# Kernel tuning notes

Hardware: AMD Instinct MI355X
Metric: run time of the kernel (lower is better)

## Reference

```python
import jax, jax.numpy as jnp
import numpy as np
import math

E = 16          # num_experts
TOP_K = 2       # num_experts_per_tok (used as capacity_factor in EC routing)
D = 1024        # embed_dim
F = 4096        # expert_hidden_dim = mlp_ratio * D
SH = 2048       # shared intermediate = F * n_shared_experts // mlp_ratio


def setup_inputs() -> dict:
    key = jax.random.key(0)
    ks = jax.random.split(key, 10)
    s = lambda k, shape, fan: jax.random.normal(k, shape, jnp.float32) / np.sqrt(fan)
    return {
        "x": jax.random.normal(ks[0], (32, 256, D), jnp.float32),
        "gate_w": s(ks[1], (E, D), D),                 # ECMoEGate.weight
        "up_w": s(ks[2], (E, F, D), D),                # fused_up.weight
        "up_b": s(ks[3], (E, F), D),                   # fused_up.bias
        "gw": s(ks[4], (E, F, D), D),                  # fused_gate.weight
        "gb": s(ks[5], (E, F), D),                     # fused_gate.bias
        "down_w": s(ks[6], (E, D, F), F),              # fused_down.weight
        "down_b": s(ks[7], (E, D), F),                 # fused_down.bias
        "sh_gate_w": s(ks[8], (SH, D), D),             # shared_experts.gate_proj
        "sh_up_w": s(ks[9], (SH, D), D),               # shared_experts.up_proj
        "sh_down_w": s(jax.random.fold_in(key, 11), (D, SH), SH),  # shared_experts.down_proj
    }


def reference(x, gate_w, up_w, up_b, gw, gb, down_w, down_b, sh_gate_w, sh_up_w, sh_down_w):
    B, S, Dm = x.shape
    h = x.reshape(-1, Dm)                               # [T, D]
    T = h.shape[0]
    # gate: sigmoid scores, expert-choice top-k over tokens per expert
    scores = jax.nn.sigmoid(h @ gate_w.T)               # [T, E]
    cap = math.ceil(T / E * TOP_K)                      # capacity per expert
    topk_score, topk_ids = jax.lax.top_k(scores.T, cap) # [E, cap]
    # dispatch: gather tokens per expert
    xin = h[topk_ids]                                   # [E, cap, D]
    # batched expert GLU (baddbmm equivalent)
    up = jnp.einsum('ecd,efd->ecf', xin, up_w) + up_b[:, None, :]
    g = jnp.einsum('ecd,efd->ecf', xin, gw) + gb[:, None, :]
    eo = jax.nn.silu(g) * up                            # [E, cap, F]
    eo = jnp.einsum('ecf,edf->ecd', eo, down_w) + down_b[:, None, :]
    # combine: weighted scatter-add back to token positions
    flat = (eo * topk_score[..., None]).reshape(-1, Dm) # [E*cap, D]
    out = jnp.zeros_like(h).at[topk_ids.reshape(-1)].add(flat)
    out = out.reshape(B, S, Dm)
    # shared dense GLU MLP (SiLU)
    shared = (jax.nn.silu(jnp.einsum('bsd,fd->bsf', x, sh_gate_w))
              * jnp.einsum('bsd,fd->bsf', x, sh_up_w))
    shared = jnp.einsum('bsf,df->bsd', shared, sh_down_w)
    return out + shared
```

## Files before the change

### kernel.cpp

```cpp
#include <hip/hip_runtime.h>
#include <hip/hip_bf16.h>

#define Tn 8192
#define Dn 1024
#define Fn 4096
#define SHn 2048
#define En 16
#define CAPn 1024

typedef __bf16 bf16_t;
typedef bf16_t bf16x8 __attribute__((ext_vector_type(8)));
typedef float f32x4 __attribute__((ext_vector_type(4)));

__device__ __forceinline__ unsigned short f2bf(float f) {
  unsigned int u = __builtin_bit_cast(unsigned int, f);
  u += 0x7FFFu + ((u >> 16) & 1u);
  return (unsigned short)(u >> 16);
}
__device__ __forceinline__ unsigned int pack2(float a, float b) {
  return (unsigned int)f2bf(a) | ((unsigned int)f2bf(b) << 16);
}

__device__ __forceinline__ void gload16(const void* g, void* l) {
  __builtin_amdgcn_global_load_lds(
      (const __attribute__((address_space(1))) unsigned int*)g,
      (__attribute__((address_space(3))) unsigned int*)l, 16, 0, 0);
}

__device__ __forceinline__ void conv_blocks(int cb, int ncb, int tid,
                                            const float* s1, unsigned short* d1, int n1,
                                            const float* s2, unsigned short* d2, int n2) {
  const int tot = n1 + n2;
  for (int i = cb * 256 + tid; i < tot; i += ncb * 256) {
    const float4* sv; uint4* dv; int j;
    if (i < n1) { j = i; sv = (const float4*)s1; dv = (uint4*)d1; }
    else        { j = i - n1; sv = (const float4*)s2; dv = (uint4*)d2; }
    float4 a = sv[2 * j], b = sv[2 * j + 1];
    dv[j] = uint4{ pack2(a.x, a.y), pack2(a.z, a.w), pack2(b.x, b.y), pack2(b.z, b.w) };
  }
}

__device__ __forceinline__ void conv4(int cb, int ncb, int tid,
                                      const float* __restrict__ s,
                                      unsigned short* __restrict__ d, int n8) {
  const int step = ncb * 256;
  const float4* sv = (const float4*)s;
  uint4* dv = (uint4*)d;
  for (int i = cb * 256 + tid; i < n8; i += 4 * step) {
    const int i1 = i + step, i2 = i + 2 * step, i3 = i + 3 * step;
    const bool v1 = i1 < n8, v2 = i2 < n8, v3 = i3 < n8;
    float4 a0 = sv[2 * i], b0 = sv[2 * i + 1];
    float4 a1{}, b1{}, a2{}, b2{}, a3{}, b3{};
    if (v1) { a1 = sv[2 * i1]; b1 = sv[2 * i1 + 1]; }
    if (v2) { a2 = sv[2 * i2]; b2 = sv[2 * i2 + 1]; }
    if (v3) { a3 = sv[2 * i3]; b3 = sv[2 * i3 + 1]; }
    dv[i] = uint4{ pack2(a0.x, a0.y), pack2(a0.z, a0.w), pack2(b0.x, b0.y), pack2(b0.z, b0.w) };
    if (v1) dv[i1] = uint4{ pack2(a1.x, a1.y), pack2(a1.z, a1.w), pack2(b1.x, b1.y), pack2(b1.z, b1.w) };
    if (v2) dv[i2] = uint4{ pack2(a2.x, a2.y), pack2(a2.z, a2.w), pack2(b2.x, b2.y), pack2(b2.z, b2.w) };
    if (v3) dv[i3] = uint4{ pack2(a3.x, a3.y), pack2(a3.z, a3.w), pack2(b3.x, b3.y), pack2(b3.z, b3.w) };
  }
}

__global__ __launch_bounds__(256) void kscores_cvt(
    const float* __restrict__ x, const float* __restrict__ gw,
    float* __restrict__ sc, unsigned short* __restrict__ xb,
    const float* __restrict__ shg, unsigned short* __restrict__ shgb,
    const float* __restrict__ shu, unsigned short* __restrict__ shub,
    const float* __restrict__ shd, unsigned short* __restrict__ shdb) {
  __shared__ float sx[Dn];
  const int tid = threadIdx.x;
  if (blockIdx.x >= Tn) {
    const int cb = blockIdx.x - Tn, ncb = gridDim.x - Tn;
    constexpr int nsh = SHn * Dn / 8;
    conv_blocks(cb, ncb, tid, shg, shgb, nsh, shu, shub, nsh);
    conv_blocks(cb, ncb, tid, shd, shdb, nsh, nullptr, nullptr, 0);
    return;
  }
  const int tok = blockIdx.x;
  float4 v = ((const float4*)(x + (size_t)tok * Dn))[tid];
  ((float4*)sx)[tid] = v;
  ((uint2*)(xb + (size_t)tok * Dn))[tid] = uint2{ pack2(v.x, v.y), pack2(v.z, v.w) };
  __syncthreads();
  int e = tid >> 4, kl = tid & 15;
  const float4* w = (const float4*)(gw + e * Dn);
  const float4* xv = (const float4*)sx;
  float acc = 0.f;
#pragma unroll
  for (int j = 0; j < 16; ++j) {
    float4 a = w[kl + 16 * j], b = xv[kl + 16 * j];
    acc += a.x * b.x + a.y * b.y + a.z * b.z + a.w * b.w;
  }
#pragma unroll
  for (int off = 8; off; off >>= 1) acc += __shfl_xor(acc, off, 64);
  if (kl == 0) sc[(size_t)e * Tn + tok] = 1.f / (1.f + expf(-acc));
}

__global__ __launch_bounds__(256) void kselect(const float* __restrict__ scores,
                                               int* __restrict__ ids,
                                               float* __restrict__ oscore) {
  __shared__ unsigned int keys[Tn];
  __shared__ unsigned int hist[256];
  __shared__ unsigned int sh_prefix, sh_k, sh_cnt, sh_eq;
  __shared__ int eqlist[1024];
  const int tid = threadIdx.x, e = blockIdx.x;
  const float* row = scores + (size_t)e * Tn;
  for (int i = 0; i < Tn / 256; ++i)
    keys[tid + i * 256] = __float_as_uint(row[tid + i * 256]);
  if (tid == 0) { sh_prefix = 0u; sh_k = CAPn; }
  __syncthreads();
  for (int shift = 24; shift >= 0; shift -= 8) {
    hist[tid] = 0u;
    __syncthreads();
    unsigned int prefix = sh_prefix;
    unsigned int mask = (shift == 24) ? 0u : (0xFFFFFFFFu << (shift + 8));
    for (int i = 0; i < Tn / 256; ++i) {
      unsigned int kk = keys[tid + i * 256];
      if ((kk & mask) == prefix) atomicAdd(&hist[(kk >> shift) & 255], 1u);
    }
    __syncthreads();
    if (tid == 0) {
      unsigned int k = sh_k, c = 0; int b;
      for (b = 255; b >= 0; --b) { c += hist[b]; if (c >= k) break; }
      sh_k = k - (c - hist[b]);
      sh_prefix = prefix | ((unsigned int)b << shift);
    }
    __syncthreads();
  }
  const unsigned int thr = sh_prefix;
  if (tid == 0) { sh_cnt = 0u; sh_eq = 0u; }
  __syncthreads();
  const int base = e * CAPn;
  for (int i = 0; i < Tn / 256; ++i) {
    int t = tid + i * 256;
    unsigned int kk = keys[t];
    if (kk > thr) {
      unsigned int p = atomicAdd(&sh_cnt, 1u);
      ids[base + p] = t;
      oscore[base + p] = __uint_as_float(kk);
    } else if (kk == thr) {
      unsigned int p = atomicAdd(&sh_eq, 1u);
      if (p < 1024u) eqlist[p] = t;
    }
  }
  __syncthreads();
  if (tid == 0) {
    int need = CAPn - (int)sh_cnt;
    int m = (int)sh_eq; if (m > 1024) m = 1024;
    for (int j = 0; j < need; ++j) {
      int best = 1 << 30, bi = 0;
      for (int i2 = 0; i2 < m; ++i2)
        if (eqlist[i2] < best) { best = eqlist[i2]; bi = i2; }
      eqlist[bi] = 1 << 30;
      ids[base + (int)sh_cnt + j] = best;
      oscore[base + (int)sh_cnt + j] = __uint_as_float(thr);
    }
  }
}


template <bool GATHER>
__global__ __launch_bounds__(256, 2) void kglu_bf(
    const unsigned short* __restrict__ X, const int* __restrict__ idsg,
    const unsigned short* __restrict__ Wg, const unsigned short* __restrict__ Wu,
    const float* __restrict__ biasg, const float* __restrict__ biasu,
    unsigned short* __restrict__ H, int N, int Mz, int MB, int NB,
    int gemmN, int convP,
    const float* __restrict__ cS1, unsigned short* __restrict__ cD1, int cn1) {
  constexpr int K = Dn;
  __shared__ alignas(16) unsigned char sA[16384];
  __shared__ alignas(16) unsigned char sB1[16384];
  __shared__ alignas(16) unsigned char sB2[16384];
  __shared__ int sIds[128];
  const int tid = threadIdx.x;
  const int bid = blockIdx.x;
  if (convP && (bid % convP) == convP - 1) {
    conv4(bid / convP, gridDim.x - gemmN, tid, cS1, cD1, cn1);
    return;
  }
  const int gbid = convP ? (bid - bid / convP) : bid;
  const int cpx = gemmN >> 3;
  const int swz = (gbid & 7) * cpx + (gbid >> 3);
  const int bm = swz % MB;
  const int bn = (swz / MB) % NB;
  const int z  = swz / (MB * NB);
  const int lane = tid & 63, w = tid >> 6;
  const int wm = w >> 1, wn = w & 1;
  const int lrow = lane & 15, lk = lane >> 4;
  const int row0 = bm * 128;

  if (tid < 128) sIds[tid] = GATHER ? idsg[z * CAPn + row0 + tid] : (row0 + tid);
  __syncthreads();

  const int lr = lane >> 3;
  const int lc = lane & 7;
  const int srcb = ((lc ^ lr) << 4);
  const unsigned char* Xb = (const unsigned char*)X;
  const unsigned char* Gb = (const unsigned char*)Wg + (size_t)z * N * (K * 2);
  const unsigned char* Ub = (const unsigned char*)Wu + (size_t)z * N * (K * 2);
  const unsigned char* aP[4];
#pragma unroll
  for (int i = 0; i < 4; ++i) {
    int ar = w * 32 + 8 * i + lr;
    aP[i] = Xb + (size_t)sIds[ar] * (K * 2) + srcb;
  }
  const int br0 = bn * 128 + w * 32 + lr;
  const unsigned char* gP0 = Gb + (size_t)br0 * (K * 2) + srcb;
  const unsigned char* uP0 = Ub + (size_t)br0 * (K * 2) + srcb;

  f32x4 accG[4][4], accU[4][4];
#pragma unroll
  for (int m = 0; m < 4; ++m)
#pragma unroll
    for (int n = 0; n < 4; ++n) {
      accG[m][n] = {0.f, 0.f, 0.f, 0.f};
      accU[m][n] = {0.f, 0.f, 0.f, 0.f};
    }

  for (int k0b = 0; k0b < K * 2; k0b += 128) {
    __syncthreads();
#pragma unroll
    for (int i = 0; i < 4; ++i) {
      unsigned ldsoff = (unsigned)(w * 32 + 8 * i) * 128u;
      gload16(aP[i] + k0b, sA + ldsoff);
      gload16(gP0 + (size_t)i * 8 * (K * 2) + k0b, sB1 + ldsoff);
      gload16(uP0 + (size_t)i * 8 * (K * 2) + k0b, sB2 + ldsoff);
    }
    __syncthreads();
#pragma unroll
    for (int ks = 0; ks < 2; ++ks) {
      const int swb = (((ks * 4 + lk) ^ (lrow & 7)) << 4);
      bf16x8 av[4], gv[4], uv[4];
#pragma unroll
      for (int m = 0; m < 4; ++m)
        av[m] = *(const bf16x8*)(sA + (wm * 64 + m * 16 + lrow) * 128 + swb);
#pragma unroll
      for (int n = 0; n < 4; ++n) {
        gv[n] = *(const bf16x8*)(sB1 + (wn * 64 + n * 16 + lrow) * 128 + swb);
        uv[n] = *(const bf16x8*)(sB2 + (wn * 64 + n * 16 + lrow) * 128 + swb);
      }
#pragma unroll
      for (int m = 0; m < 4; ++m)
#pragma unroll
        for (int n = 0; n < 4; ++n) {
          accG[m][n] = __builtin_amdgcn_mfma_f32_16x16x32_bf16(av[m], gv[n], accG[m][n], 0, 0, 0);
          accU[m][n] = __builtin_amdgcn_mfma_f32_16x16x32_bf16(av[m], uv[n], accU[m][n], 0, 0, 0);
        }
    }
  }
#pragma unroll
  for (int n = 0; n < 4; ++n) {
    int col = bn * 128 + wn * 64 + n * 16 + lrow;
    float bg = biasg ? biasg[(size_t)z * N + col] : 0.f;
    float bu = biasu ? biasu[(size_t)z * N + col] : 0.f;
#pragma unroll
    for (int m = 0; m < 4; ++m) {
#pragma unroll
      for (int j = 0; j < 4; ++j) {
        float g = accG[m][n][j] + bg;
        float u = accU[m][n][j] + bu;
        float h = g / (1.f + __expf(-g)) * u;
        int row = row0 + wm * 64 + m * 16 + lk * 4 + j;
        H[(size_t)z * Mz * N + (size_t)row * N + col] = f2bf(h);
      }
    }
  }
}

template <int K, bool SCATTER>
__global__ __launch_bounds__(256, 2) void kdown_bf(
    const unsigned short* __restrict__ Hin, const unsigned short* __restrict__ W,
    const float* __restrict__ bias, const int* __restrict__ idsg,
    const float* __restrict__ scg, float* __restrict__ Out, int Mz, int MB, int NB,
    int gemmN, int convP,
    const float* __restrict__ cS1, unsigned short* __restrict__ cD1, int cn1) {
  constexpr int N = Dn;
  __shared__ alignas(16) unsigned char sA[16384];
  __shared__ alignas(16) unsigned char sB[16384];
  __shared__ int sIds[128];
  __shared__ float sSc[128];
  const int tid = threadIdx.x;
  const int bid = blockIdx.x;
  if (convP && (bid % convP) == convP - 1) {
    conv4(bid / convP, gridDim.x - gemmN, tid, cS1, cD1, cn1);
    return;
  }
  const int gbid = convP ? (bid - bid / convP) : bid;
  const int cpx = gemmN >> 3;
  const int swz = (gbid & 7) * cpx + (gbid >> 3);
  const int bm = swz % MB;
  const int bn = (swz / MB) % NB;
  const int z  = swz / (MB * NB);
  const int lane = tid & 63, w = tid >> 6;
  const int wm = w >> 1, wn = w & 1;
  const int lrow = lane & 15, lk = lane >> 4;
  const int row0 = bm * 128;

  if (SCATTER && tid < 128) {
    sIds[tid] = idsg[z * CAPn + row0 + tid];
    sSc[tid] = scg[z * CAPn + row0 + tid];
  }
  __syncthreads();

  const int lr = lane >> 3;
  const int lc = lane & 7;
  const int srcb = ((lc ^ lr) << 4);
  const unsigned char* Ab = (const unsigned char*)Hin + (size_t)z * Mz * (K * 2);
  const unsigned char* Wb = (const unsigned char*)W + (size_t)z * N * (K * 2);
  const int ar0 = row0 + w * 32 + lr;
  const int br0 = bn * 128 + w * 32 + lr;
  const unsigned char* aP0 = Ab + (size_t)ar0 * (K * 2) + srcb;
  const unsigned char* bP0 = Wb + (size_t)br0 * (K * 2) + srcb;

  f32x4 acc[4][4];
#pragma unroll
  for (int m = 0; m < 4; ++m)
#pragma unroll
    for (int n = 0; n < 4; ++n) acc[m][n] = {0.f, 0.f, 0.f, 0.f};

  for (int k0b = 0; k0b < K * 2; k0b += 128) {
    __syncthreads();
#pragma unroll
    for (int i = 0; i < 4; ++i) {
      unsigned ldsoff = (unsigned)(w * 32 + 8 * i) * 128u;
      gload16(aP0 + (size_t)i * 8 * (K * 2) + k0b, sA + ldsoff);
      gload16(bP0 + (size_t)i * 8 * (K * 2) + k0b, sB + ldsoff);
    }
    __syncthreads();
#pragma unroll
    for (int ks = 0; ks < 2; ++ks) {
      const int swb = (((ks * 4 + lk) ^ (lrow & 7)) << 4);
      bf16x8 av[4], bv[4];
#pragma unroll
      for (int m = 0; m < 4; ++m)
        av[m] = *(const bf16x8*)(sA + (wm * 64 + m * 16 + lrow) * 128 + swb);
#pragma unroll
      for (int n = 0; n < 4; ++n)
        bv[n] = *(const bf16x8*)(sB + (wn * 64 + n * 16 + lrow) * 128 + swb);
#pragma unroll
      for (int m = 0; m < 4; ++m)
#pragma unroll
        for (int n = 0; n < 4; ++n)
          acc[m][n] = __builtin_amdgcn_mfma_f32_16x16x32_bf16(av[m], bv[n], acc[m][n], 0, 0, 0);
    }
  }
#pragma unroll
  for (int n = 0; n < 4; ++n) {
    int col = bn * 128 + wn * 64 + n * 16 + lrow;
    float bvv = bias ? bias[(size_t)z * N + col] : 0.f;
#pragma unroll
    for (int m = 0; m < 4; ++m) {
#pragma unroll
      for (int j = 0; j < 4; ++j) {
        int rl = wm * 64 + m * 16 + lk * 4 + j;
        float v = acc[m][n][j] + bvv;
        if (SCATTER) {
          atomicAdd(Out + (size_t)sIds[rl] * Dn + col, sSc[rl] * v);
        } else {
          Out[(size_t)(row0 + rl) * Dn + col] = v;
        }
      }
    }
  }
}

__global__ __launch_bounds__(256, 2) void kdown256(
    const unsigned short* __restrict__ Hin, const unsigned short* __restrict__ W,
    const float* __restrict__ bias, const int* __restrict__ idsg,
    const float* __restrict__ scg, float* __restrict__ Out) {
  constexpr int K = Fn;
  constexpr int N = Dn;
  constexpr int MB = CAPn / 128;
  constexpr int NB = Dn / 256;
  __shared__ alignas(16) unsigned char sA[16384];
  __shared__ alignas(16) unsigned char sB[32768];
  __shared__ int sIds[128];
  __shared__ float sSc[128];
  const int tid = threadIdx.x;
  const int bid = blockIdx.x;
  const int cpx = gridDim.x >> 3;
  const int swz = (bid & 7) * cpx + (bid >> 3);
  const int bm = swz % MB;
  const int bn = (swz / MB) % NB;
  const int z  = swz / (MB * NB);
  const int lane = tid & 63, w = tid >> 6;
  const int wm = w >> 1, wn = w & 1;
  const int lrow = lane & 15, lk = lane >> 4;
  const int row0 = bm * 128;

  if (tid < 128) {
    sIds[tid] = idsg[z * CAPn + row0 + tid];
    sSc[tid] = scg[z * CAPn + row0 + tid];
  }
  __syncthreads();

  const int lr = lane >> 3;
  const int lc = lane & 7;
  const int srcb = ((lc ^ lr) << 4);
  const unsigned char* Ab = (const unsigned char*)Hin + (size_t)z * CAPn * (K * 2);
  const unsigned char* Wb = (const unsigned char*)W + (size_t)z * N * (K * 2);
  const int ar0 = row0 + w * 32 + lr;
  const int br0 = bn * 256 + w * 64 + lr;
  const unsigned char* aP0 = Ab + (size_t)ar0 * (K * 2) + srcb;
  const unsigned char* bP0 = Wb + (size_t)br0 * (K * 2) + srcb;

  f32x4 acc[4][8];
#pragma unroll
  for (int m = 0; m < 4; ++m)
#pragma unroll
    for (int n = 0; n < 8; ++n) acc[m][n] = {0.f, 0.f, 0.f, 0.f};

  for (int k0b = 0; k0b < K * 2; k0b += 128) {
    __syncthreads();
#pragma unroll
    for (int i = 0; i < 4; ++i)
      gload16(aP0 + (size_t)i * 8 * (K * 2) + k0b,
              sA + (unsigned)(w * 32 + 8 * i) * 128u);
#pragma unroll
    for (int i = 0; i < 8; ++i)
      gload16(bP0 + (size_t)i * 8 * (K * 2) + k0b,
              sB + (unsigned)(w * 64 + 8 * i) * 128u);
    __syncthreads();
#pragma unroll
    for (int ks = 0; ks < 2; ++ks) {
      const int swb = (((ks * 4 + lk) ^ (lrow & 7)) << 4);
      bf16x8 av[4], bv[8];
#pragma unroll
      for (int m = 0; m < 4; ++m)
        av[m] = *(const bf16x8*)(sA + (wm * 64 + m * 16 + lrow) * 128 + swb);
#pragma unroll
      for (int n = 0; n < 8; ++n)
        bv[n] = *(const bf16x8*)(sB + (wn * 128 + n * 16 + lrow) * 128 + swb);
#pragma unroll
      for (int m = 0; m < 4; ++m)
#pragma unroll
        for (int n = 0; n < 8; ++n)
          acc[m][n] = __builtin_amdgcn_mfma_f32_16x16x32_bf16(av[m], bv[n], acc[m][n], 0, 0, 0);
    }
  }
#pragma unroll
  for (int n = 0; n < 8; ++n) {
    int col = bn * 256 + wn * 128 + n * 16 + lrow;
    float bvv = bias[(size_t)z * N + col];
#pragma unroll
    for (int m = 0; m < 4; ++m) {
#pragma unroll
      for (int j = 0; j < 4; ++j) {
        int rl = wm * 64 + m * 16 + lk * 4 + j;
        atomicAdd(Out + (size_t)sIds[rl] * Dn + col, sSc[rl] * (acc[m][n][j] + bvv));
      }
    }
  }
}

extern "C" void kernel_launch(void* const* d_in, const int* in_sizes, int n_in,
                              void* d_out, int out_size, void* d_ws, size_t ws_size,
                              hipStream_t stream) {
  const float* x      = (const float*)d_in[0];
  const float* gate_w = (const float*)d_in[1];
  const float* up_w   = (const float*)d_in[2];
  const float* up_b   = (const float*)d_in[3];
  const float* gw     = (const float*)d_in[4];
  const float* gb     = (const float*)d_in[5];
  const float* down_w = (const float*)d_in[6];
  const float* down_b = (const float*)d_in[7];
  const float* shg    = (const float*)d_in[8];
  const float* shu    = (const float*)d_in[9];
  const float* shd    = (const float*)d_in[10];
  float* out = (float*)d_out;

  const size_t H_BYTES  = (size_t)En * CAPn * Fn * 2;
  const size_t XB_BYTES = (size_t)Tn * Dn * 2;
  const size_t WE_BYTES = (size_t)En * Fn * Dn * 2;
  const size_t SH_BYTES = (size_t)SHn * Dn * 2;
  const size_t SC_BYTES = (size_t)En * Tn * 4;
  const size_t ID_BYTES = (size_t)En * CAPn * 4;
  const size_t need = H_BYTES + XB_BYTES + 3 * WE_BYTES + 3 * SH_BYTES +
                      SC_BYTES + 2 * ID_BYTES;
  if (ws_size < need) return;

  char* p = (char*)d_ws;
  unsigned short* H    = (unsigned short*)p; p += H_BYTES;
  unsigned short* xb   = (unsigned short*)p; p += XB_BYTES;
  unsigned short* upb  = (unsigned short*)p; p += WE_BYTES;
  unsigned short* gwb  = (unsigned short*)p; p += WE_BYTES;
  unsigned short* dwb  = (unsigned short*)p; p += WE_BYTES;
  unsigned short* shgb = (unsigned short*)p; p += SH_BYTES;
  unsigned short* shub = (unsigned short*)p; p += SH_BYTES;
  unsigned short* shdb = (unsigned short*)p; p += SH_BYTES;
  float* scores = (float*)p; p += SC_BYTES;
  int* ids      = (int*)p;  p += ID_BYTES;
  float* osc    = (float*)p;

  constexpr int NWE8 = En * Fn * Dn / 8;

  kscores_cvt<<<Tn + 256, 256, 0, stream>>>(x, gate_w, scores, xb,
                                            shg, shgb, shu, shub, shd, shdb);
  kselect<<<En, 256, 0, stream>>>(scores, ids, osc);

  kglu_bf<false><<<1024 + 1024, 256, 0, stream>>>(
      xb, nullptr, shgb, shub, nullptr, nullptr, H, SHn, Tn, Tn / 128, SHn / 128,
      1024, 2, up_w, upb, NWE8);

  kdown_bf<SHn, false><<<512 + 512, 256, 0, stream>>>(
      H, shdb, nullptr, nullptr, nullptr, out, Tn, Tn / 128, Dn / 128,
      512, 2, gw, gwb, NWE8);

  kglu_bf<true><<<4096 + 1024, 256, 0, stream>>>(
      xb, ids, gwb, upb, gb, up_b, H, Fn, CAPn, CAPn / 128, Fn / 128,
      4096, 5, down_w, dwb, NWE8);

  kdown256<<<(CAPn / 128) * (Dn / 256) * En, 256, 0, stream>>>(
      H, dwb, down_b, ids, osc, out);
}
```

Measured before the change: 934.4 us.

## Move expert weight bf16 conversion into the scores kernel and drop interleaved conversion

```diff
diff --git a/kernel.cpp b/kernel.cpp
--- a/kernel.cpp
+++ b/kernel.cpp
@@ -62,8 +62,11 @@
 }
 
 __global__ __launch_bounds__(256) void kscores_cvt(
-    const float* __restrict__ x, const float* __restrict__ gw,
+    const float* __restrict__ x, const float* __restrict__ gatew,
     float* __restrict__ sc, unsigned short* __restrict__ xb,
+    const float* __restrict__ upw, unsigned short* __restrict__ upb,
+    const float* __restrict__ gw, unsigned short* __restrict__ gwb,
+    const float* __restrict__ dw, unsigned short* __restrict__ dwb,
     const float* __restrict__ shg, unsigned short* __restrict__ shgb,
     const float* __restrict__ shu, unsigned short* __restrict__ shub,
     const float* __restrict__ shd, unsigned short* __restrict__ shdb) {
@@ -71,7 +74,11 @@
   const int tid = threadIdx.x;
   if (blockIdx.x >= Tn) {
     const int cb = blockIdx.x - Tn, ncb = gridDim.x - Tn;
+    constexpr int NWE8 = En * Fn * Dn / 8;
     constexpr int nsh = SHn * Dn / 8;
+    conv4(cb, ncb, tid, upw, upb, NWE8);
+    conv4(cb, ncb, tid, gw, gwb, NWE8);
+    conv4(cb, ncb, tid, dw, dwb, NWE8);
     conv_blocks(cb, ncb, tid, shg, shgb, nsh, shu, shub, nsh);
     conv_blocks(cb, ncb, tid, shd, shdb, nsh, nullptr, nullptr, 0);
     return;
@@ -82,7 +89,7 @@
   ((uint2*)(xb + (size_t)tok * Dn))[tid] = uint2{ pack2(v.x, v.y), pack2(v.z, v.w) };
   __syncthreads();
   int e = tid >> 4, kl = tid & 15;
-  const float4* w = (const float4*)(gw + e * Dn);
+  const float4* w = (const float4*)(gatew + e * Dn);
   const float4* xv = (const float4*)sx;
   float acc = 0.f;
 #pragma unroll
@@ -163,9 +170,7 @@
     const unsigned short* __restrict__ X, const int* __restrict__ idsg,
     const unsigned short* __restrict__ Wg, const unsigned short* __restrict__ Wu,
     const float* __restrict__ biasg, const float* __restrict__ biasu,
-    unsigned short* __restrict__ H, int N, int Mz, int MB, int NB,
-    int gemmN, int convP,
-    const float* __restrict__ cS1, unsigned short* __restrict__ cD1, int cn1) {
+    unsigned short* __restrict__ H, int N, int Mz, int MB, int NB) {
   constexpr int K = Dn;
   __shared__ alignas(16) unsigned char sA[16384];
   __shared__ alignas(16) unsigned char sB1[16384];
@@ -173,13 +178,8 @@
   __shared__ int sIds[128];
   const int tid = threadIdx.x;
   const int bid = blockIdx.x;
-  if (convP && (bid % convP) == convP - 1) {
-    conv4(bid / convP, gridDim.x - gemmN, tid, cS1, cD1, cn1);
-    return;
-  }
-  const int gbid = convP ? (bid - bid / convP) : bid;
-  const int cpx = gemmN >> 3;
-  const int swz = (gbid & 7) * cpx + (gbid >> 3);
+  const int cpx = gridDim.x >> 3;
+  const int swz = (bid & 7) * cpx + (bid >> 3);
   const int bm = swz % MB;
   const int bn = (swz / MB) % NB;
   const int z  = swz / (MB * NB);
@@ -266,27 +266,17 @@
   }
 }
 
-template <int K, bool SCATTER>
+template <int K>
 __global__ __launch_bounds__(256, 2) void kdown_bf(
     const unsigned short* __restrict__ Hin, const unsigned short* __restrict__ W,
-    const float* __restrict__ bias, const int* __restrict__ idsg,
-    const float* __restrict__ scg, float* __restrict__ Out, int Mz, int MB, int NB,
-    int gemmN, int convP,
-    const float* __restrict__ cS1, unsigned short* __restrict__ cD1, int cn1) {
+    float* __restrict__ Out, int Mz, int MB, int NB) {
   constexpr int N = Dn;
   __shared__ alignas(16) unsigned char sA[16384];
   __shared__ alignas(16) unsigned char sB[16384];
-  __shared__ int sIds[128];
-  __shared__ float sSc[128];
   const int tid = threadIdx.x;
   const int bid = blockIdx.x;
-  if (convP && (bid % convP) == convP - 1) {
-    conv4(bid / convP, gridDim.x - gemmN, tid, cS1, cD1, cn1);
-    return;
-  }
-  const int gbid = convP ? (bid - bid / convP) : bid;
-  const int cpx = gemmN >> 3;
-  const int swz = (gbid & 7) * cpx + (gbid >> 3);
+  const int cpx = gridDim.x >> 3;
+  const int swz = (bid & 7) * cpx + (bid >> 3);
   const int bm = swz % MB;
   const int bn = (swz / MB) % NB;
   const int z  = swz / (MB * NB);
@@ -294,12 +284,6 @@
   const int wm = w >> 1, wn = w & 1;
   const int lrow = lane & 15, lk = lane >> 4;
   const int row0 = bm * 128;
-
-  if (SCATTER && tid < 128) {
-    sIds[tid] = idsg[z * CAPn + row0 + tid];
-    sSc[tid] = scg[z * CAPn + row0 + tid];
-  }
-  __syncthreads();
 
   const int lr = lane >> 3;
   const int lc = lane & 7;
@@ -346,18 +330,12 @@
 #pragma unroll
   for (int n = 0; n < 4; ++n) {
     int col = bn * 128 + wn * 64 + n * 16 + lrow;
-    float bvv = bias ? bias[(size_t)z * N + col] : 0.f;
 #pragma unroll
     for (int m = 0; m < 4; ++m) {
 #pragma unroll
       for (int j = 0; j < 4; ++j) {
         int rl = wm * 64 + m * 16 + lk * 4 + j;
-        float v = acc[m][n][j] + bvv;
-        if (SCATTER) {
-          atomicAdd(Out + (size_t)sIds[rl] * Dn + col, sSc[rl] * v);
-        } else {
-          Out[(size_t)(row0 + rl) * Dn + col] = v;
-        }
+        Out[(size_t)(row0 + rl) * Dn + col] = acc[m][n][j];
       }
     }
   }
@@ -491,23 +469,19 @@
   int* ids      = (int*)p;  p += ID_BYTES;
   float* osc    = (float*)p;
 
-  constexpr int NWE8 = En * Fn * Dn / 8;
-
-  kscores_cvt<<<Tn + 256, 256, 0, stream>>>(x, gate_w, scores, xb,
-                                            shg, shgb, shu, shub, shd, shdb);
+  kscores_cvt<<<Tn + 2048, 256, 0, stream>>>(x, gate_w, scores, xb,
+                                             up_w, upb, gw, gwb, down_w, dwb,
+                                             shg, shgb, shu, shub, shd, shdb);
   kselect<<<En, 256, 0, stream>>>(scores, ids, osc);
 
-  kglu_bf<false><<<1024 + 1024, 256, 0, stream>>>(
-      xb, nullptr, shgb, shub, nullptr, nullptr, H, SHn, Tn, Tn / 128, SHn / 128,
-      1024, 2, up_w, upb, NWE8);
-
-  kdown_bf<SHn, false><<<512 + 512, 256, 0, stream>>>(
-      H, shdb, nullptr, nullptr, nullptr, out, Tn, Tn / 128, Dn / 128,
-      512, 2, gw, gwb, NWE8);
-
-  kglu_bf<true><<<4096 + 1024, 256, 0, stream>>>(
-      xb, ids, gwb, upb, gb, up_b, H, Fn, CAPn, CAPn / 128, Fn / 128,
-      4096, 5, down_w, dwb, NWE8);
+  kglu_bf<false><<<(Tn / 128) * (SHn / 128), 256, 0, stream>>>(
+      xb, nullptr, shgb, shub, nullptr, nullptr, H, SHn, Tn, Tn / 128, SHn / 128);
+
+  kdown_bf<SHn><<<(Tn / 128) * (Dn / 128), 256, 0, stream>>>(
+      H, shdb, out, Tn, Tn / 128, Dn / 128);
+
+  kglu_bf<true><<<(CAPn / 128) * (Fn / 128) * En, 256, 0, stream>>>(
+      xb, ids, gwb, upb, gb, up_b, H, Fn, CAPn, CAPn / 128, Fn / 128);
 
   kdown256<<<(CAPn / 128) * (Dn / 256) * En, 256, 0, stream>>>(
       H, dwb, down_b, ids, osc, out);
```

Measured after the change: 973.6 us. +4.2%, slower.
